# Performance work log

Hardware: AMD Instinct MI355X
Metric: run time of the kernel (lower is better)

The kernel has to match this reference:

```python
import jax, jax.numpy as jnp
import numpy as np


def setup_inputs() -> dict:
    key = jax.random.key(0)
    ks = jax.random.split(key, 5)
    t, b, s, d = 4, 4, 1024, 512
    x = jax.random.normal(ks[0], (t, b, s, d), dtype=jnp.float32)
    wq = jax.random.normal(ks[1], (d, d), dtype=jnp.float32) * 0.02
    wk = jax.random.normal(ks[2], (d, d), dtype=jnp.float32) * 0.02
    wv = jax.random.normal(ks[3], (d, d), dtype=jnp.float32) * 0.02
    wo = jax.random.normal(ks[4], (d, d), dtype=jnp.float32) * 0.02
    z = jnp.zeros((d,), dtype=jnp.float32)
    return {"x": x, "wq": wq, "bq": z, "wk": wk, "bk": z, "wv": wv,
            "bv": z, "wo": wo, "bo": z, "num_heads": 8}


def reference(x, wq, bq, wk, bk, wv, bv, wo, bo, num_heads):
    t, b, s, d = x.shape
    dh = d // num_heads
    # QKV projections (torch Linear stores weight as [out,in]; here weights are
    # random square matrices so x @ w + b is the same math)
    q = x @ wq + bq
    k = x @ wk + bk
    v = x @ wv + bv
    # Faithful to source: plain row-major view to (t*b*h, s, dh) WITHOUT
    # transposing a head axis (this mixes seq blocks into the batch-of-heads dim)
    q = q.reshape(t * b * num_heads, s, dh)
    k = k.reshape(t * b * num_heads, s, dh)
    v = v.reshape(t * b * num_heads, s, dh)
    scale = 1.0 / jnp.sqrt(jnp.float32(dh))
    scores = jnp.einsum('bqd,bkd->bqk', q, k) * scale  # [t*b*h, s, s]
    attn = jax.nn.softmax(scores, axis=-1)
    out = jnp.einsum('bqk,bkd->bqd', attn, v)  # [t*b*h, s, dh]
    out = out.reshape(t, b, s, d)
    return out @ wo + bo
```

## Files before the change

kernel.cpp:

```cpp
#include <hip/hip_runtime.h>

typedef __bf16 bf16;
typedef __bf16 bf16x4 __attribute__((ext_vector_type(4)));
typedef __bf16 bf16x8 __attribute__((ext_vector_type(8)));
typedef float  f32x4  __attribute__((ext_vector_type(4)));
typedef float  f32x16 __attribute__((ext_vector_type(16)));
typedef unsigned int u32x4 __attribute__((ext_vector_type(4)));

#define MFMA16(a, b, c) __builtin_amdgcn_mfma_f32_16x16x32_bf16((a), (b), (c), 0, 0, 0)
#define MFMA32(a, b, c) __builtin_amdgcn_mfma_f32_32x32x16_bf16((a), (b), (c), 0, 0, 0)
#define SW(row, g) (((row) << 6) + ((((g) ^ ((row) & 7))) << 3))

#define QSCALE 0.1803368801111137f

typedef __attribute__((address_space(3))) uint32_t       lds_u32_t;
typedef const __attribute__((address_space(1))) uint32_t glob_u32_t;

__device__ __forceinline__ void ld_lds16(const bf16* g, bf16* l) {
    __builtin_amdgcn_global_load_lds((glob_u32_t*)g, (lds_u32_t*)l, 16, 0, 0);
}

__global__ __launch_bounds__(256) void prep(
    const float* __restrict__ X,
    const float* __restrict__ wq, const float* __restrict__ wk,
    const float* __restrict__ wv, const float* __restrict__ wo,
    bf16* __restrict__ Xb, bf16* __restrict__ wqkvT, bf16* __restrict__ woT)
{
    int bid = blockIdx.x;
    if (bid < 4096) {
        size_t i = ((size_t)bid * 256 + threadIdx.x) * 8;
        const f32x4* s = (const f32x4*)(X + i);
        f32x4 a = s[0], b = s[1];
        bf16x8 o;
        for (int e = 0; e < 4; e++) { o[e] = (bf16)a[e]; o[e + 4] = (bf16)b[e]; }
        *(bf16x8*)(Xb + i) = o;
    } else {
        int idx = (bid - 4096) * 256 + threadIdx.x;
        int which = idx >> 15;
        int r = idx & 32767;
        int kg = r >> 9, n = r & 511;
        const float* w = (which == 0) ? wq : (which == 1) ? wk : (which == 2) ? wv : wo;
        bf16x8 o;
        for (int e = 0; e < 8; e++) o[e] = (bf16)w[(size_t)(kg * 8 + e) * 512 + n];
        bf16* dst = ((which < 3) ? (wqkvT + (size_t)which * 262144) : woT) + (size_t)n * 512 + kg * 8;
        *(bf16x8*)dst = o;
    }
}

__global__ __launch_bounds__(256, 4) void gemm_qkv(
    const bf16* __restrict__ Xb, const bf16* __restrict__ WT,
    const float* __restrict__ bq, const float* __restrict__ bk,
    const float* __restrict__ bv,
    bf16* __restrict__ Q, bf16* __restrict__ K, bf16* __restrict__ V)
{
    __shared__ char smem[34816];
    bf16* As = (bf16*)smem;
    bf16* Bs = (bf16*)(smem + 16384);

    const int t = threadIdx.x;
    const int lane = t & 63, wid = t >> 6;
    const int wr = wid >> 1, wc = wid & 1;
    const int lr = lane & 15, quad = lane >> 4;
    const int bid = blockIdx.x;
    const int xcd = bid & 7, j0 = bid >> 3;
    const int m0 = (xcd * 16 + (j0 & 15)) * 128;
    const int x = j0 >> 4;
    const int which = x >> 2;
    const int n0 = (x & 3) * 128;
    const bf16* Wt = WT + (size_t)which * 262144;

    f32x4 zf = {0.f, 0.f, 0.f, 0.f};
    f32x4 acc[4][4];
    for (int i = 0; i < 4; i++)
        for (int jj = 0; jj < 4; jj++) acc[i][jj] = zf;

    const int srow = t >> 3;
    const int sg = (t & 7) ^ (srow & 7);
    const bf16* gA = Xb + (size_t)(m0 + srow) * 512 + sg * 8;
    const bf16* gB = Wt + (size_t)(n0 + srow) * 512 + sg * 8;
    bf16* lA = As + t * 8;
    bf16* lB = Bs + t * 8;

    for (int k0 = 0; k0 < 512; k0 += 64) {
        for (int p = 0; p < 4; p++) {
            ld_lds16(gA + k0 + p * 32 * 512, lA + p * 2048);
            ld_lds16(gB + k0 + p * 32 * 512, lB + p * 2048);
        }
        __syncthreads();
        for (int kk = 0; kk < 2; ++kk) {
            bf16x8 af[4], bf_[4];
            for (int i = 0; i < 4; i++)
                af[i] = *(const bf16x8*)&As[SW(wr * 64 + i * 16 + lr, kk * 4 + quad)];
            for (int jj = 0; jj < 4; jj++)
                bf_[jj] = *(const bf16x8*)&Bs[SW(wc * 64 + jj * 16 + lr, kk * 4 + quad)];
            for (int i = 0; i < 4; i++)
                for (int jj = 0; jj < 4; jj++)
                    acc[i][jj] = MFMA16(af[i], bf_[jj], acc[i][jj]);
        }
        __syncthreads();
    }

    bf16* OUT = (which == 0) ? Q : (which == 1) ? K : V;
    const float* bias = (which == 0) ? bq : (which == 1) ? bk : bv;
    const float qs = (which == 0) ? QSCALE : 1.0f;

    bf16* Ep = (bf16*)smem + wid * 4352;
    for (int jj = 0; jj < 4; jj++) {
        int n = n0 + wc * 64 + jj * 16 + lr;
        float bb = bias[n];
        for (int i = 0; i < 4; i++) {
            int row = i * 16 + quad * 4;
            for (int r = 0; r < 4; r++)
                Ep[(row + r) * 68 + jj * 16 + lr] = (bf16)((acc[i][jj][r] + bb) * qs);
        }
    }
    bf16* wO = OUT + (size_t)(m0 + wr * 64) * 512 + n0 + wc * 64;
    for (int s = 0; s < 8; s++) {
        int row = s * 8 + (lane >> 3), g = lane & 7;
        *(bf16x8*)(wO + (size_t)row * 512 + g * 8) = *(const bf16x8*)&Ep[row * 68 + g * 8];
    }
}

__global__ __launch_bounds__(256, 4) void gemm_out(
    const bf16* __restrict__ A, const bf16* __restrict__ WoT,
    const float* __restrict__ bo, float* __restrict__ OUT)
{
    __shared__ char smem[34816];
    bf16* As = (bf16*)smem;
    bf16* Bs = (bf16*)(smem + 16384);

    const int t = threadIdx.x;
    const int lane = t & 63, wid = t >> 6;
    const int wr = wid >> 1, wc = wid & 1;
    const int lr = lane & 15, quad = lane >> 4;
    const int bid = blockIdx.x;
    const int xcd = bid & 7, j0 = bid >> 3;
    const int m0 = (xcd * 16 + (j0 & 15)) * 128;
    const int n0 = (j0 >> 4) * 128;

    f32x4 zf = {0.f, 0.f, 0.f, 0.f};
    f32x4 acc[4][4];
    for (int i = 0; i < 4; i++)
        for (int jj = 0; jj < 4; jj++) acc[i][jj] = zf;

    const int srow = t >> 3;
    const int sg = (t & 7) ^ (srow & 7);
    const bf16* gA = A + (size_t)(m0 + srow) * 512 + sg * 8;
    const bf16* gB = WoT + (size_t)(n0 + srow) * 512 + sg * 8;
    bf16* lA = As + t * 8;
    bf16* lB = Bs + t * 8;

    for (int k0 = 0; k0 < 512; k0 += 64) {
        for (int p = 0; p < 4; p++) {
            ld_lds16(gA + k0 + p * 32 * 512, lA + p * 2048);
            ld_lds16(gB + k0 + p * 32 * 512, lB + p * 2048);
        }
        __syncthreads();
        for (int kk = 0; kk < 2; ++kk) {
            bf16x8 af[4], bf_[4];
            for (int i = 0; i < 4; i++)
                af[i] = *(const bf16x8*)&As[SW(wr * 64 + i * 16 + lr, kk * 4 + quad)];
            for (int jj = 0; jj < 4; jj++)
                bf_[jj] = *(const bf16x8*)&Bs[SW(wc * 64 + jj * 16 + lr, kk * 4 + quad)];
            for (int i = 0; i < 4; i++)
                for (int jj = 0; jj < 4; jj++)
                    acc[i][jj] = MFMA16(af[i], bf_[jj], acc[i][jj]);
        }
        __syncthreads();
    }

    float bb[4];
    for (int jj = 0; jj < 4; jj++) bb[jj] = bo[n0 + wc * 64 + jj * 16 + lr];

    float* Ef = (float*)smem + wid * 2112;
    for (int h = 0; h < 2; h++) {
        for (int jj = 0; jj < 4; jj++)
            for (int ii = 0; ii < 2; ii++) {
                int i = h * 2 + ii;
                int row = ii * 16 + quad * 4;
                for (int r = 0; r < 4; r++)
                    Ef[(row + r) * 66 + jj * 16 + lr] = acc[i][jj][r] + bb[jj];
            }
        float* wO = OUT + (size_t)(m0 + wr * 64 + h * 32) * 512 + n0 + wc * 64;
        for (int s = 0; s < 8; s++) {
            int row = s * 4 + (lane >> 4), c = (lane & 15) * 4;
            *(f32x4*)(wO + (size_t)row * 512 + c) = *(const f32x4*)&Ef[row * 66 + c];
        }
        __syncthreads();
    }
}

__global__ __launch_bounds__(256) void transpose_v(
    const bf16* __restrict__ V, bf16* __restrict__ VT)
{
    __shared__ bf16 L[64 * 72];
    const int t = threadIdx.x;
    const int b = blockIdx.y, kb = blockIdx.x;
    const bf16* src = V + ((size_t)b * 1024 + (size_t)kb * 64) * 64;
    const int row = t >> 2, c0 = (t & 3) * 16;
    *(bf16x8*)&L[row * 72 + c0]     = *(const bf16x8*)(src + row * 64 + c0);
    *(bf16x8*)&L[row * 72 + c0 + 8] = *(const bf16x8*)(src + row * 64 + c0 + 8);
    __syncthreads();
    bf16x8 o0, o1;
    for (int e = 0; e < 8; e++) {
        o0[e] = L[(c0 + e) * 72 + row];
        o1[e] = L[(c0 + 8 + e) * 72 + row];
    }
    bf16* dst = VT + ((size_t)b * 64 + row) * 1024 + (size_t)kb * 64 + c0;
    *(bf16x8*)dst       = o0;
    *(bf16x8*)(dst + 8) = o1;
}

__global__ __launch_bounds__(256, 4) void attn(
    const bf16* __restrict__ Q, const bf16* __restrict__ K,
    const bf16* __restrict__ VT, bf16* __restrict__ O)
{
    __shared__ char smem[32768];
    bf16* const K0 = (bf16*)smem;
    bf16* const V0 = (bf16*)(smem + 8192);
    bf16* const K1 = (bf16*)(smem + 16384);
    bf16* const V1 = (bf16*)(smem + 24576);

    const int t = threadIdx.x, lane = t & 63, wid = t >> 6;
    const int q31 = lane & 31, hi = lane >> 5;
    const int bid = blockIdx.x;
    const int batch = (bid & 7) * 16 + ((bid >> 3) & 15);
    const int q0 = (bid >> 7) * 128;
    const bf16* Qb = Q + (size_t)batch * 65536;
    const bf16* Kb = K + (size_t)batch * 65536;
    const bf16* Vb = VT + (size_t)batch * 65536;

    bf16x8 qf[4];
#pragma unroll
    for (int kk = 0; kk < 4; ++kk)
        qf[kk] = *(const bf16x8*)(Qb + (size_t)(q0 + wid * 32 + q31) * 64 + kk * 16 + hi * 8);

    f32x16 oacc[2];
#pragma unroll
    for (int ct = 0; ct < 2; ++ct)
#pragma unroll
        for (int r = 0; r < 16; ++r) oacc[ct][r] = 0.f;
    float lsum = 0.f;

    const int srow = t >> 3;
    const int sg8 = ((t & 7) ^ (srow & 7)) * 8;

#define STAGE(ktile, KD, VD) do {                                        \
        const bf16* gK_ = Kb + (size_t)(ktile) * 4096;                   \
        const bf16* gV_ = Vb + (size_t)(ktile) * 64;                     \
        ld_lds16(gK_ + srow * 64 + sg8,                  (KD) + t * 8);  \
        ld_lds16(gK_ + (srow + 32) * 64 + sg8,           (KD) + t * 8 + 2048); \
        ld_lds16(gV_ + (size_t)srow * 1024 + sg8,        (VD) + t * 8);  \
        ld_lds16(gV_ + (size_t)(srow + 32) * 1024 + sg8, (VD) + t * 8 + 2048); \
    } while (0)

    STAGE(0, K0, V0);

    for (int kt = 0; kt < 16; ++kt) {
        bf16* Kt = (kt & 1) ? K1 : K0;
        bf16* Vt = (kt & 1) ? V1 : V0;
        bf16* Kn = (kt & 1) ? K0 : K1;
        bf16* Vn = (kt & 1) ? V0 : V1;

        __builtin_amdgcn_sched_barrier(0);
        __builtin_amdgcn_s_barrier();
        __builtin_amdgcn_sched_barrier(0);
        if (kt < 15) {
            STAGE(kt + 1, Kn, Vn);
            asm volatile("s_waitcnt vmcnt(4)" ::: "memory");
        } else {
            asm volatile("s_waitcnt vmcnt(0)" ::: "memory");
        }
        __builtin_amdgcn_sched_barrier(0);
        __builtin_amdgcn_s_barrier();
        __builtin_amdgcn_sched_barrier(0);

        f32x16 sacc[2];
#pragma unroll
        for (int i2 = 0; i2 < 2; ++i2)
#pragma unroll
            for (int r = 0; r < 16; ++r) sacc[i2][r] = 0.f;

        __builtin_amdgcn_s_setprio(1);
#pragma unroll
        for (int kk = 0; kk < 4; ++kk) {
            bf16x8 a0 = *(const bf16x8*)&Kt[SW(q31, kk * 2 + hi)];
            bf16x8 a1 = *(const bf16x8*)&Kt[SW(32 + q31, kk * 2 + hi)];
            sacc[0] = MFMA32(a0, qf[kk], sacc[0]);
            sacc[1] = MFMA32(a1, qf[kk], sacc[1]);
        }
        __builtin_amdgcn_s_setprio(0);

        float ls = 0.f;
#pragma unroll
        for (int i2 = 0; i2 < 2; ++i2)
#pragma unroll
            for (int r = 0; r < 16; ++r) {
                float p = __builtin_amdgcn_exp2f(sacc[i2][r]);
                ls += p;
                sacc[i2][r] = p;
            }
        lsum += ls;

        bf16x8 pa[4];
#pragma unroll
        for (int c = 0; c < 4; ++c) {
            const int i2 = c >> 1, rb = (c & 1) * 8;
            uint32_t x0, x1, x2, x3;
            asm("v_cvt_pk_bf16_f32 %0, %1, %2" : "=v"(x0) : "v"(sacc[i2][rb + 0]), "v"(sacc[i2][rb + 1]));
            asm("v_cvt_pk_bf16_f32 %0, %1, %2" : "=v"(x1) : "v"(sacc[i2][rb + 2]), "v"(sacc[i2][rb + 3]));
            asm("v_cvt_pk_bf16_f32 %0, %1, %2" : "=v"(x2) : "v"(sacc[i2][rb + 4]), "v"(sacc[i2][rb + 5]));
            asm("v_cvt_pk_bf16_f32 %0, %1, %2" : "=v"(x3) : "v"(sacc[i2][rb + 6]), "v"(sacc[i2][rb + 7]));
            asm volatile("v_permlane32_swap_b32 %0, %1" : "+v"(x0), "+v"(x2));
            asm volatile("v_permlane32_swap_b32 %0, %1" : "+v"(x1), "+v"(x3));
            u32x4 w = {x0, x1, x2, x3};
            pa[c] = __builtin_bit_cast(bf16x8, w);
        }

        __builtin_amdgcn_s_setprio(1);
#pragma unroll
        for (int c = 0; c < 4; ++c)
#pragma unroll
            for (int ct = 0; ct < 2; ++ct) {
                bf16x8 bv = *(const bf16x8*)&Vt[SW(ct * 32 + q31, c * 2 + hi)];
                oacc[ct] = MFMA32(pa[c], bv, oacc[ct]);
            }
        __builtin_amdgcn_s_setprio(0);
    }
#undef STAGE

    lsum += __shfl_xor(lsum, 32, 64);
    const float invl = 1.f / lsum;

    __syncthreads();
    bf16* Ep = (bf16*)smem + wid * 2176;
#pragma unroll
    for (int r = 0; r < 16; ++r) {
        const int ql = (r & 3) + 8 * (r >> 2) + 4 * hi;
        const float im = __shfl(invl, ql, 64);
        Ep[ql * 68 + q31]      = (bf16)(oacc[0][r] * im);
        Ep[ql * 68 + 32 + q31] = (bf16)(oacc[1][r] * im);
    }
    bf16* Ob = O + (size_t)batch * 65536 + (size_t)(q0 + wid * 32) * 64;
#pragma unroll
    for (int s = 0; s < 4; s++) {
        int row = s * 8 + (lane >> 3), g = lane & 7;
        *(bf16x8*)(Ob + (size_t)row * 64 + g * 8) = *(const bf16x8*)&Ep[row * 68 + g * 8];
    }
}

extern "C" void kernel_launch(void* const* d_in, const int* in_sizes, int n_in,
                              void* d_out, int out_size, void* d_ws, size_t ws_size,
                              hipStream_t stream)
{
    const float* x  = (const float*)d_in[0];
    const float* wq = (const float*)d_in[1];
    const float* bq = (const float*)d_in[2];
    const float* wk = (const float*)d_in[3];
    const float* bk = (const float*)d_in[4];
    const float* wv = (const float*)d_in[5];
    const float* bv = (const float*)d_in[6];
    const float* wo = (const float*)d_in[7];
    const float* bo = (const float*)d_in[8];

    char* ws = (char*)d_ws;
    bf16* wqkvT = (bf16*)ws;
    bf16* woT   = (bf16*)(ws + 1572864);
    bf16* Xb    = (bf16*)(ws + 2097152);
    bf16* VTb   = Xb;
    bf16* Qb    = (bf16*)(ws + 2097152 + 16777216ull);
    bf16* Kb    = (bf16*)(ws + 2097152 + 2 * 16777216ull);
    bf16* Vb    = (bf16*)(ws + 2097152 + 3 * 16777216ull);
    bf16* Ab    = Vb;

    prep<<<4608, 256, 0, stream>>>(x, wq, wk, wv, wo, Xb, wqkvT, woT);
    gemm_qkv<<<1536, 256, 0, stream>>>(Xb, wqkvT, bq, bk, bv, Qb, Kb, Vb);
    transpose_v<<<dim3(16, 128), 256, 0, stream>>>(Vb, VTb);
    attn<<<1024, 256, 0, stream>>>(Qb, Kb, VTb, Ab);
    gemm_out<<<512, 256, 0, stream>>>(Ab, woT, bo, (float*)d_out);
}
```

Baseline: 202.5 us.

## Double-buffer LDS tiles in QKV and output projection GEMMs

Both projection GEMMs now use two 32 KB LDS buffers and issue the global-to-LDS loads for the next K-tile before computing on the current one. Explicit vmcnt waits and barriers replace the load-then-sync pattern, so memory latency can overlap with MFMA work. The cost is doubled LDS per block (64 KB), with launch bounds lowered from 4 to 2 blocks per CU, which reduces occupancy.

Result: slower. 211.3 us (+4.4%).

```diff
diff --git a/kernel.cpp b/kernel.cpp
--- a/kernel.cpp
+++ b/kernel.cpp
@@ -47,15 +47,13 @@
     }
 }
 
-__global__ __launch_bounds__(256, 4) void gemm_qkv(
+__global__ __launch_bounds__(256, 2) void gemm_qkv(
     const bf16* __restrict__ Xb, const bf16* __restrict__ WT,
     const float* __restrict__ bq, const float* __restrict__ bk,
     const float* __restrict__ bv,
     bf16* __restrict__ Q, bf16* __restrict__ K, bf16* __restrict__ V)
 {
-    __shared__ char smem[34816];
-    bf16* As = (bf16*)smem;
-    bf16* Bs = (bf16*)(smem + 16384);
+    __shared__ char smem[65536];
 
     const int t = threadIdx.x;
     const int lane = t & 63, wid = t >> 6;
@@ -78,15 +76,34 @@
     const int sg = (t & 7) ^ (srow & 7);
     const bf16* gA = Xb + (size_t)(m0 + srow) * 512 + sg * 8;
     const bf16* gB = Wt + (size_t)(n0 + srow) * 512 + sg * 8;
-    bf16* lA = As + t * 8;
-    bf16* lB = Bs + t * 8;
-
-    for (int k0 = 0; k0 < 512; k0 += 64) {
-        for (int p = 0; p < 4; p++) {
-            ld_lds16(gA + k0 + p * 32 * 512, lA + p * 2048);
-            ld_lds16(gB + k0 + p * 32 * 512, lB + p * 2048);
-        }
-        __syncthreads();
+
+#define GSTAGE(k0, b) do {                                               \
+        bf16* lA_ = (bf16*)(smem + (b) * 32768) + t * 8;                 \
+        bf16* lB_ = (bf16*)(smem + (b) * 32768 + 16384) + t * 8;         \
+        for (int p = 0; p < 4; p++) {                                    \
+            ld_lds16(gA + (k0) + p * 32 * 512, lA_ + p * 2048);          \
+            ld_lds16(gB + (k0) + p * 32 * 512, lB_ + p * 2048);          \
+        }                                                                \
+    } while (0)
+
+    GSTAGE(0, 0);
+#pragma unroll
+    for (int kt = 0; kt < 8; ++kt) {
+        __builtin_amdgcn_sched_barrier(0);
+        __builtin_amdgcn_s_barrier();
+        __builtin_amdgcn_sched_barrier(0);
+        if (kt < 7) {
+            GSTAGE((kt + 1) * 64, (kt + 1) & 1);
+            asm volatile("s_waitcnt vmcnt(8)" ::: "memory");
+        } else {
+            asm volatile("s_waitcnt vmcnt(0)" ::: "memory");
+        }
+        __builtin_amdgcn_sched_barrier(0);
+        __builtin_amdgcn_s_barrier();
+        __builtin_amdgcn_sched_barrier(0);
+
+        const bf16* As = (const bf16*)(smem + (kt & 1) * 32768);
+        const bf16* Bs = As + 8192;
         for (int kk = 0; kk < 2; ++kk) {
             bf16x8 af[4], bf_[4];
             for (int i = 0; i < 4; i++)
@@ -97,12 +114,14 @@
                 for (int jj = 0; jj < 4; jj++)
                     acc[i][jj] = MFMA16(af[i], bf_[jj], acc[i][jj]);
         }
-        __syncthreads();
-    }
+    }
+#undef GSTAGE
 
     bf16* OUT = (which == 0) ? Q : (which == 1) ? K : V;
     const float* bias = (which == 0) ? bq : (which == 1) ? bk : bv;
     const float qs = (which == 0) ? QSCALE : 1.0f;
+
+    __syncthreads();
 
     bf16* Ep = (bf16*)smem + wid * 4352;
     for (int jj = 0; jj < 4; jj++) {
@@ -121,13 +140,11 @@
     }
 }
 
-__global__ __launch_bounds__(256, 4) void gemm_out(
+__global__ __launch_bounds__(256, 2) void gemm_out(
     const bf16* __restrict__ A, const bf16* __restrict__ WoT,
     const float* __restrict__ bo, float* __restrict__ OUT)
 {
-    __shared__ char smem[34816];
-    bf16* As = (bf16*)smem;
-    bf16* Bs = (bf16*)(smem + 16384);
+    __shared__ char smem[65536];
 
     const int t = threadIdx.x;
     const int lane = t & 63, wid = t >> 6;
@@ -147,15 +164,34 @@
     const int sg = (t & 7) ^ (srow & 7);
     const bf16* gA = A + (size_t)(m0 + srow) * 512 + sg * 8;
     const bf16* gB = WoT + (size_t)(n0 + srow) * 512 + sg * 8;
-    bf16* lA = As + t * 8;
-    bf16* lB = Bs + t * 8;
-
-    for (int k0 = 0; k0 < 512; k0 += 64) {
-        for (int p = 0; p < 4; p++) {
-            ld_lds16(gA + k0 + p * 32 * 512, lA + p * 2048);
-            ld_lds16(gB + k0 + p * 32 * 512, lB + p * 2048);
-        }
-        __syncthreads();
+
+#define GSTAGE(k0, b) do {                                               \
+        bf16* lA_ = (bf16*)(smem + (b) * 32768) + t * 8;                 \
+        bf16* lB_ = (bf16*)(smem + (b) * 32768 + 16384) + t * 8;         \
+        for (int p = 0; p < 4; p++) {                                    \
+            ld_lds16(gA + (k0) + p * 32 * 512, lA_ + p * 2048);          \
+            ld_lds16(gB + (k0) + p * 32 * 512, lB_ + p * 2048);          \
+        }                                                                \
+    } while (0)
+
+    GSTAGE(0, 0);
+#pragma unroll
+    for (int kt = 0; kt < 8; ++kt) {
+        __builtin_amdgcn_sched_barrier(0);
+        __builtin_amdgcn_s_barrier();
+        __builtin_amdgcn_sched_barrier(0);
+        if (kt < 7) {
+            GSTAGE((kt + 1) * 64, (kt + 1) & 1);
+            asm volatile("s_waitcnt vmcnt(8)" ::: "memory");
+        } else {
+            asm volatile("s_waitcnt vmcnt(0)" ::: "memory");
+        }
+        __builtin_amdgcn_sched_barrier(0);
+        __builtin_amdgcn_s_barrier();
+        __builtin_amdgcn_sched_barrier(0);
+
+        const bf16* As = (const bf16*)(smem + (kt & 1) * 32768);
+        const bf16* Bs = As + 8192;
         for (int kk = 0; kk < 2; ++kk) {
             bf16x8 af[4], bf_[4];
             for (int i = 0; i < 4; i++)
@@ -166,11 +202,13 @@
                 for (int jj = 0; jj < 4; jj++)
                     acc[i][jj] = MFMA16(af[i], bf_[jj], acc[i][jj]);
         }
-        __syncthreads();
-    }
+    }
+#undef GSTAGE
 
     float bb[4];
     for (int jj = 0; jj < 4; jj++) bb[jj] = bo[n0 + wc * 64 + jj * 16 + lr];
+
+    __syncthreads();
 
     float* Ef = (float*)smem + wid * 2112;
     for (int h = 0; h < 2; h++) {
```

## Drop V transpose kernel; read V via LDS transpose loads in attention

Applied to the files above, without the earlier changes.

Removes the separate transpose_v kernel and loads V row-major into LDS with a custom layout. The P·V operand is then read with ds_read_b64_tr_b16 transposing loads. This saves a full read/write pass over V (16 MB) and one kernel launch. In exchange, the LDS address mapping and the new waitcnt placement must be exactly right, and the attention output buffer is remapped to the Xb region.

Result: slower. 213.3 us (+5.3%).

```diff
diff --git a/kernel.cpp b/kernel.cpp
--- a/kernel.cpp
+++ b/kernel.cpp
@@ -5,6 +5,7 @@
 typedef __bf16 bf16x8 __attribute__((ext_vector_type(8)));
 typedef float  f32x4  __attribute__((ext_vector_type(4)));
 typedef float  f32x16 __attribute__((ext_vector_type(16)));
+typedef unsigned int u32x2 __attribute__((ext_vector_type(2)));
 typedef unsigned int u32x4 __attribute__((ext_vector_type(4)));
 
 #define MFMA16(a, b, c) __builtin_amdgcn_mfma_f32_16x16x32_bf16((a), (b), (c), 0, 0, 0)
@@ -18,6 +19,14 @@
 
 __device__ __forceinline__ void ld_lds16(const bf16* g, bf16* l) {
     __builtin_amdgcn_global_load_lds((glob_u32_t*)g, (lds_u32_t*)l, 16, 0, 0);
+}
+
+template<int OFF>
+__device__ __forceinline__ u32x2 tr_b16(uint32_t va) {
+    u32x2 d;
+    asm volatile("ds_read_b64_tr_b16 %0, %1 offset:%2"
+                 : "=v"(d) : "v"(va), "n"(OFF));
+    return d;
 }
 
 __global__ __launch_bounds__(256) void prep(
@@ -190,30 +199,9 @@
     }
 }
 
-__global__ __launch_bounds__(256) void transpose_v(
-    const bf16* __restrict__ V, bf16* __restrict__ VT)
-{
-    __shared__ bf16 L[64 * 72];
-    const int t = threadIdx.x;
-    const int b = blockIdx.y, kb = blockIdx.x;
-    const bf16* src = V + ((size_t)b * 1024 + (size_t)kb * 64) * 64;
-    const int row = t >> 2, c0 = (t & 3) * 16;
-    *(bf16x8*)&L[row * 72 + c0]     = *(const bf16x8*)(src + row * 64 + c0);
-    *(bf16x8*)&L[row * 72 + c0 + 8] = *(const bf16x8*)(src + row * 64 + c0 + 8);
-    __syncthreads();
-    bf16x8 o0, o1;
-    for (int e = 0; e < 8; e++) {
-        o0[e] = L[(c0 + e) * 72 + row];
-        o1[e] = L[(c0 + 8 + e) * 72 + row];
-    }
-    bf16* dst = VT + ((size_t)b * 64 + row) * 1024 + (size_t)kb * 64 + c0;
-    *(bf16x8*)dst       = o0;
-    *(bf16x8*)(dst + 8) = o1;
-}
-
 __global__ __launch_bounds__(256, 4) void attn(
     const bf16* __restrict__ Q, const bf16* __restrict__ K,
-    const bf16* __restrict__ VT, bf16* __restrict__ O)
+    const bf16* __restrict__ V, bf16* __restrict__ O)
 {
     __shared__ char smem[32768];
     bf16* const K0 = (bf16*)smem;
@@ -228,7 +216,7 @@
     const int q0 = (bid >> 7) * 128;
     const bf16* Qb = Q + (size_t)batch * 65536;
     const bf16* Kb = K + (size_t)batch * 65536;
-    const bf16* Vb = VT + (size_t)batch * 65536;
+    const bf16* Vb = V + (size_t)batch * 65536;
 
     bf16x8 qf[4];
 #pragma unroll
@@ -244,23 +232,28 @@
 
     const int srow = t >> 3;
     const int sg8 = ((t & 7) ^ (srow & 7)) * 8;
+    const int vkey = ((t >> 5) << 2) | ((t >> 1) & 3);
+    const int vdh  = (((t >> 3) & 3) << 4) | ((t & 1) << 3);
 
 #define STAGE(ktile, KD, VD) do {                                        \
         const bf16* gK_ = Kb + (size_t)(ktile) * 4096;                   \
-        const bf16* gV_ = Vb + (size_t)(ktile) * 64;                     \
-        ld_lds16(gK_ + srow * 64 + sg8,                  (KD) + t * 8);  \
-        ld_lds16(gK_ + (srow + 32) * 64 + sg8,           (KD) + t * 8 + 2048); \
-        ld_lds16(gV_ + (size_t)srow * 1024 + sg8,        (VD) + t * 8);  \
-        ld_lds16(gV_ + (size_t)(srow + 32) * 1024 + sg8, (VD) + t * 8 + 2048); \
+        const bf16* gV_ = Vb + (size_t)(ktile) * 4096;                   \
+        ld_lds16(gK_ + srow * 64 + sg8,          (KD) + t * 8);          \
+        ld_lds16(gK_ + (srow + 32) * 64 + sg8,   (KD) + t * 8 + 2048);   \
+        ld_lds16(gV_ + vkey * 64 + vdh,          (VD) + t * 8);          \
+        ld_lds16(gV_ + (vkey + 32) * 64 + vdh,   (VD) + t * 8 + 2048);   \
     } while (0)
+
+    const uint32_t vaL = ((uint32_t)hi << 10) + (((lane >> 4) & 1) << 7) + ((lane & 15) << 3);
+    const uint32_t vaV0 = vaL + 8192u, vaV1 = vaL + 24576u;
 
     STAGE(0, K0, V0);
 
     for (int kt = 0; kt < 16; ++kt) {
         bf16* Kt = (kt & 1) ? K1 : K0;
-        bf16* Vt = (kt & 1) ? V1 : V0;
         bf16* Kn = (kt & 1) ? K0 : K1;
         bf16* Vn = (kt & 1) ? V0 : V1;
+        const uint32_t va = (kt & 1) ? vaV1 : vaV0;
 
         __builtin_amdgcn_sched_barrier(0);
         __builtin_amdgcn_s_barrier();
@@ -290,6 +283,17 @@
             sacc[1] = MFMA32(a1, qf[kk], sacc[1]);
         }
         __builtin_amdgcn_s_setprio(0);
+
+        u32x2 tv[4][2][2];
+#define TRPAIR(c, ct) do {                                               \
+        tv[c][ct][0] = tr_b16<(c) * 2048 + (ct) * 256>(va);              \
+        tv[c][ct][1] = tr_b16<(c) * 2048 + (ct) * 256 + 512>(va);        \
+    } while (0)
+        TRPAIR(0, 0); TRPAIR(0, 1);
+        TRPAIR(1, 0); TRPAIR(1, 1);
+        TRPAIR(2, 0); TRPAIR(2, 1);
+        TRPAIR(3, 0); TRPAIR(3, 1);
+#undef TRPAIR
 
         float ls = 0.f;
 #pragma unroll
@@ -317,13 +321,16 @@
             pa[c] = __builtin_bit_cast(bf16x8, w);
         }
 
+        asm volatile("s_waitcnt lgkmcnt(0)" ::: "memory");
+        __builtin_amdgcn_sched_barrier(0);
         __builtin_amdgcn_s_setprio(1);
 #pragma unroll
         for (int c = 0; c < 4; ++c)
 #pragma unroll
             for (int ct = 0; ct < 2; ++ct) {
-                bf16x8 bv = *(const bf16x8*)&Vt[SW(ct * 32 + q31, c * 2 + hi)];
-                oacc[ct] = MFMA32(pa[c], bv, oacc[ct]);
+                u32x4 w = {tv[c][ct][0][0], tv[c][ct][0][1],
+                           tv[c][ct][1][0], tv[c][ct][1][1]};
+                oacc[ct] = MFMA32(pa[c], __builtin_bit_cast(bf16x8, w), oacc[ct]);
             }
         __builtin_amdgcn_s_setprio(0);
     }
@@ -367,15 +374,13 @@
     bf16* wqkvT = (bf16*)ws;
     bf16* woT   = (bf16*)(ws + 1572864);
     bf16* Xb    = (bf16*)(ws + 2097152);
-    bf16* VTb   = Xb;
     bf16* Qb    = (bf16*)(ws + 2097152 + 16777216ull);
     bf16* Kb    = (bf16*)(ws + 2097152 + 2 * 16777216ull);
     bf16* Vb    = (bf16*)(ws + 2097152 + 3 * 16777216ull);
-    bf16* Ab    = Vb;
+    bf16* Ab    = Xb;
 
     prep<<<4608, 256, 0, stream>>>(x, wq, wk, wv, wo, Xb, wqkvT, woT);
     gemm_qkv<<<1536, 256, 0, stream>>>(Xb, wqkvT, bq, bk, bv, Qb, Kb, Vb);
-    transpose_v<<<dim3(16, 128), 256, 0, stream>>>(Vb, VTb);
-    attn<<<1024, 256, 0, stream>>>(Qb, Kb, VTb, Ab);
+    attn<<<1024, 256, 0, stream>>>(Qb, Kb, Vb, Ab);
     gemm_out<<<512, 256, 0, stream>>>(Ab, woT, bo, (float*)d_out);
 }
```
